# Kernel tuning notes

Measured on AMD Instinct MI355X. Metric: run time of the kernel, lower is better.

The kernel has to match this reference:

```python
import jax, jax.numpy as jnp
import numpy as np

N_E = 1792      # 7 * 256, forced by n_e // 7 == 256 slice width
E_DIM = 64
BETA = 0.25
SUB = 256       # sub-codebook size selected by pos


def setup_inputs() -> dict:
    key = jax.random.key(0)
    k1, k2, k3 = jax.random.split(key, 3)
    z = jax.random.normal(k1, (16, 16384, E_DIM), dtype=jnp.float32)
    one_hot = jax.random.normal(k2, (7,), dtype=jnp.float32)
    W = jax.random.uniform(k3, (N_E, E_DIM), dtype=jnp.float32,
                           minval=-1.0 / N_E, maxval=1.0 / N_E)
    return {"z": z, "one_hot": one_hot, "W": W}


def reference(z, one_hot, W):
    B, T, D = z.shape
    zf = z.reshape(-1, D)                      # [N, D]
    pos = jnp.argmax(one_hot)                  # which 256-entry sub-codebook
    E = jax.lax.dynamic_slice(W, (pos * SUB, 0), (SUB, D))  # [256, D]

    # pairwise squared distances: ||z||^2 + ||e||^2 - 2 z.e
    d = (jnp.sum(zf * zf, axis=1, keepdims=True)
         + jnp.sum(E * E, axis=1)
         - 2.0 * zf @ E.T)                     # [N, 256]
    idx = jnp.argmin(d, axis=1)                # [N]

    # quantize: one-hot @ E == gather (same math, no [N,256] one-hot in HBM)
    z_q = E[idx].reshape(z.shape)              # [B, T, D]

    sg = jax.lax.stop_gradient
    loss = (BETA * jnp.mean((sg(z_q) - z) ** 2)
            + jnp.mean((z_q - sg(z)) ** 2))

    z_q_st = z + sg(z_q - z)                   # straight-through

    # e_mean = column mean of the one-hot matrix == normalized bincount
    counts = jax.ops.segment_sum(jnp.ones_like(idx, jnp.float32), idx,
                                 num_segments=SUB)
    e_mean = counts / idx.shape[0]
    perplexity = jnp.exp(-jnp.sum(e_mean * jnp.log(e_mean + 1e-10)))

    z_q_out = jnp.transpose(z_q_st, (0, 2, 1))  # [B, D, T]
    return (z_q_out, loss, perplexity, idx[:, None])
```

## Files before the change

### kernel.cpp

```cpp
#include <hip/hip_runtime.h>

#define NROWS (16*16384)
#define NJ 256
#define NBLK 1024
#define OUT_LOSS 16777216
#define OUT_PERP 16777217
#define OUT_IDX  16777218

typedef float f32x4  __attribute__((ext_vector_type(4)));
typedef float f32x16 __attribute__((ext_vector_type(16)));
typedef short s16x8  __attribute__((ext_vector_type(8)));

__device__ inline unsigned short f2bf(float f){
  unsigned u = __builtin_bit_cast(unsigned, f);
  unsigned r = (u + 0x7FFFu + ((u >> 16) & 1u)) >> 16;
  return (unsigned short)r;
}
__device__ inline float bf2f(unsigned short h){
  unsigned u = ((unsigned)h) << 16;
  return __builtin_bit_cast(float, u);
}


__global__ __launch_bounds__(512, 2) void vq_main(
    const float* __restrict__ z, const float* __restrict__ oh,
    const float* __restrict__ W, float* __restrict__ out,
    double* __restrict__ lossA, int* __restrict__ wsCnt4,
    unsigned* __restrict__ qn, unsigned* __restrict__ qrows, unsigned segcap)
{
  __shared__ short e1l[NJ*64];
  __shared__ short e2l[NJ*64];
  __shared__ float enl[NJ];
  __shared__ unsigned hist[NJ];
  __shared__ double sLoss[8];
  __shared__ unsigned qn_lds;

  float mv = oh[0]; int pos = 0;
  #pragma unroll
  for (int i = 1; i < 7; i++){ float v = oh[i]; if (v > mv){ mv = v; pos = i; } }

  const int tid = threadIdx.x;

  {
    const int j = tid >> 1, half = tid & 1;
    const float* Wr = W + (size_t)(pos*NJ + j)*64;
    double en = 0.0;
    #pragma unroll
    for (int s4 = 0; s4 < 4; s4++){
      const int s = half*4 + s4;
      f32x4 a = *(const f32x4*)(Wr + s*8);
      f32x4 b = *(const f32x4*)(Wr + s*8 + 4);
      s16x8 p1, p2;
      #pragma unroll
      for (int i = 0; i < 8; i++){
        float vv = (i < 4) ? a[i] : b[i-4];
        unsigned short x1 = f2bf(vv);
        float rr = vv - bf2f(x1);
        p1[i] = (short)x1;
        p2[i] = (short)f2bf(rr);
        en += (double)vv * (double)vv;
      }
      const int slot = s ^ (j & 7);
      *(s16x8*)(e1l + j*64 + slot*8) = p1;
      *(s16x8*)(e2l + j*64 + slot*8) = p2;
    }
    en += __shfl_xor(en, 1);
    if (half == 0) enl[j] = (float)en;
    if (tid < NJ) hist[tid] = 0u;
    if (tid == 0) qn_lds = 0u;
  }
  __syncthreads();

  const int w   = tid >> 6;
  const int l   = tid & 63;
  const int l31 = l & 31;
  const int lh  = l >> 5;

  const int r    = (int)blockIdx.x * 256 + w*32 + l31;
  const int b_i  = r >> 14;
  const int t    = r & 16383;
  const float* zr = z + (size_t)r * 64;

  f32x16 acc[8] = {};
  float zzp = 0.0f;
  #pragma unroll
  for (int ks = 0; ks < 4; ks++){
    const int k0 = ks*16 + lh*8;
    f32x4 za = *(const f32x4*)(zr + k0);
    f32x4 zb = *(const f32x4*)(zr + k0 + 4);
    s16x8 z1f, z2f;
    #pragma unroll
    for (int i = 0; i < 8; i++){
      float vv = (i < 4) ? za[i] : zb[i-4];
      zzp = fmaf(vv, vv, zzp);
      unsigned short x1 = f2bf(vv);
      float rr = vv - bf2f(x1);
      z1f[i] = (short)x1;
      z2f[i] = (short)f2bf(rr);
    }
    #pragma unroll
    for (int jt = 0; jt < 8; jt++){
      const int jrow = jt*32 + l31;
      const int slot = (ks*2 + lh) ^ (jrow & 7);
      const s16x8 e1f = *(const s16x8*)(e1l + jrow*64 + slot*8);
      const s16x8 e2f = *(const s16x8*)(e2l + jrow*64 + slot*8);
      acc[jt] = __builtin_amdgcn_mfma_f32_32x32x16_bf16(e1f, z1f, acc[jt], 0, 0, 0);
      acc[jt] = __builtin_amdgcn_mfma_f32_32x32x16_bf16(e1f, z2f, acc[jt], 0, 0, 0);
      acc[jt] = __builtin_amdgcn_mfma_f32_32x32x16_bf16(e2f, z1f, acc[jt], 0, 0, 0);
    }
  }
  const float zz = zzp + __shfl_xor(zzp, 32);

  float m1 = 3.4e38f, m2 = 3.4e38f; int j1 = 0;
  #pragma unroll
  for (int jt = 0; jt < 8; jt++){
    #pragma unroll
    for (int rq = 0; rq < 4; rq++){
      f32x4 en4 = *(const f32x4*)(enl + jt*32 + rq*8 + lh*4);
      #pragma unroll
      for (int q = 0; q < 4; q++){
        const int reg = rq*4 + q;
        float s  = fmaf(-2.0f, acc[jt][reg], en4[q]);
        int   jj = jt*32 + q + 8*rq + 4*lh;
        bool  lt = s < m1;
        m2 = fminf(m2, lt ? m1 : s);
        j1 = lt ? jj : j1;
        m1 = fminf(m1, s);
      }
    }
  }
  {
    float om1 = __shfl_xor(m1, 32);
    float om2 = __shfl_xor(m2, 32);
    int   oj1 = __shfl_xor(j1, 32);
    float nm2 = fminf(fminf(m2, om2), fmaxf(m1, om1));
    if (om1 < m1 || (om1 == m1 && oj1 < j1)){ m1 = om1; j1 = oj1; }
    m2 = nm2;
  }

  {
    float zs = zz*1.02f + 0.1f;
    float ub = __builtin_bit_cast(float,
                 __builtin_bit_cast(unsigned, zs) & 0x7F800000u) * 1.1920929e-7f;
    float thr = 2.0f*ub + 1.0e-6f;
    if ((m2 - m1 <= thr) && lh == 0){
      unsigned slot = atomicAdd(&qn_lds, 1u);
      if (slot < segcap)
        qrows[(size_t)blockIdx.x*segcap + slot] = (unsigned)r | ((unsigned)j1 << 18);
    }
  }

  if (lh == 0){
    out[(size_t)OUT_IDX + r] = (float)j1;
    atomicAdd(&hist[j1], 1u);
  }
  double lsum = 0.0;
  {
    const float* Er = W + (size_t)(pos*NJ + j1)*64;
    float* zq = out + (size_t)b_i * 1048576 + t;
    #pragma unroll
    for (int ks = 0; ks < 4; ks++){
      const int d0 = ks*16 + lh*8;
      f32x4 ea = *(const f32x4*)(Er + d0);
      f32x4 eb = *(const f32x4*)(Er + d0 + 4);
      f32x4 za = *(const f32x4*)(zr + d0);
      f32x4 zb = *(const f32x4*)(zr + d0 + 4);
      #pragma unroll
      for (int i = 0; i < 8; i++){
        float e  = (i < 4) ? ea[i] : eb[i-4];
        float zv = (i < 4) ? za[i] : zb[i-4];
        float df = e - zv;
        lsum = fma((double)df, (double)df, lsum);
        zq[(size_t)(d0 + i) * 16384] = zv + df;
      }
    }
  }
  #pragma unroll
  for (int off = 1; off < 64; off <<= 1) lsum += __shfl_xor(lsum, off);
  if (l == 0) sLoss[w] = lsum;
  __syncthreads();

  if (tid == 0){
    double bs = 0.0;
    #pragma unroll
    for (int i = 0; i < 8; i++) bs += sLoss[i];
    lossA[blockIdx.x] = bs;
    qn[blockIdx.x] = min(qn_lds, segcap);
  }
  if (tid < NJ){
    unsigned c = hist[tid];
    if (c) atomicAdd(wsCnt4 + ((blockIdx.x & 3) * NJ) + tid, (int)c);
  }
}

__global__ __launch_bounds__(256, 2) void vq_rescue(
    const float* __restrict__ z, const float* __restrict__ oh,
    const float* __restrict__ W, float* __restrict__ out,
    double* __restrict__ lossB, int* __restrict__ wsCnt4,
    const unsigned* __restrict__ qn, const unsigned* __restrict__ qrows,
    unsigned segcap)
{
  #pragma clang fp contract(off)
  __shared__ float elds[NJ*64];
  __shared__ float eeb[NJ];

  float mvv = oh[0]; int pos = 0;
  #pragma unroll
  for (int i = 1; i < 7; i++){ float v = oh[i]; if (v > mvv){ mvv = v; pos = i; } }
  const float* E = W + (size_t)pos * (NJ*64);

  const int tid = threadIdx.x;
  {
    const float* er = E + (size_t)tid * 64;
    float p8[8];
    #pragma unroll
    for (int k = 0; k < 8; k++){
      float ev = er[k];
      elds[tid*64 + (k ^ (tid & 31))] = ev;
      p8[k] = ev*ev;
    }
    #pragma unroll
    for (int k = 8; k < 64; k++){
      float ev = er[k];
      elds[tid*64 + (k ^ (tid & 31))] = ev;
      p8[k & 7] += ev*ev;
    }
    eeb[tid] = ((p8[0]+p8[1])+(p8[2]+p8[3]))+((p8[4]+p8[5])+(p8[6]+p8[7]));
  }
  __syncthreads();

  const int wv = tid >> 6, l = tid & 63;
  const int x  = l & 31;
  const unsigned wgid = blockIdx.x*4u + (unsigned)wv;
  const unsigned seg  = wgid >> 1;
  const unsigned sub  = wgid & 1u;
  const unsigned n    = min(qn[seg], segcap);

  double rloss = 0.0;

  for (unsigned i = sub; i < n; i += 2){
    const unsigned v = qrows[(size_t)seg*segcap + i];
    const int r    = __builtin_amdgcn_readfirstlane((int)(v & 0x3FFFFu));
    const int jold = __builtin_amdgcn_readfirstlane((int)((v >> 18) & 0xFFu));
    const float* zr = z + (size_t)r * 64;

    float zk[64];
    #pragma unroll
    for (int k = 0; k < 64; k++) zk[k] = zr[k];

    float r8[8];
    #pragma unroll
    for (int k = 0; k < 8; k++){ float p = zk[k]*zk[k]; r8[k] = p; }
    #pragma unroll
    for (int k = 8; k < 64; k++){ float p = zk[k]*zk[k]; r8[k & 7] += p; }
    const float zzs = ((r8[0]+r8[1])+(r8[2]+r8[3]))+((r8[4]+r8[5])+(r8[6]+r8[7]));

    float dbest = 3.4e38f; int jbest = 0;
    #pragma unroll
    for (int q = 0; q < 4; q++){
      const int j = l + 64*q;
      float dot = 0.0f;
      #pragma unroll
      for (int k = 0; k < 64; k++){
        float ev = elds[j*64 + (k ^ x)];
        dot = fmaf(ev, zk[k], dot);
      }
      float A  = zzs + eeb[j];
      float tw = 2.0f*dot;
      float d  = A - tw;
      if (d < dbest){ dbest = d; jbest = j; }
    }
    #pragma unroll
    for (int off = 32; off > 0; off >>= 1){
      float od = __shfl_xor(dbest, off);
      int   oj = __shfl_xor(jbest, off);
      if (od < dbest || (od == dbest && oj < jbest)){ dbest = od; jbest = oj; }
    }

    if (jbest != jold){
      const int b_i = r >> 14;
      const int t   = r & 16383;
      const float* en_ = E + (size_t)jbest * 64;
      const float* eo_ = E + (size_t)jold  * 64;
      float ze  = zr[l];
      float dfn = en_[l] - ze;
      float dfo = eo_[l] - ze;
      out[(size_t)b_i * 1048576 + (size_t)l * 16384 + t] = ze + dfn;
      double dl = (double)dfn*(double)dfn - (double)dfo*(double)dfo;
      #pragma unroll
      for (int off = 1; off < 64; off <<= 1) dl += __shfl_xor(dl, off);
      rloss += dl;
      if (l == 0){
        out[(size_t)OUT_IDX + r] = (float)jbest;
        atomicAdd(wsCnt4 + jold,  -1);
        atomicAdd(wsCnt4 + jbest,  1);
      }
    }
  }
  if (l == 0) lossB[wgid] = rloss;
}

__global__ __launch_bounds__(1024) void vq_fin(
    const double* __restrict__ lossA, const double* __restrict__ lossB,
    const int* __restrict__ wsCnt4, float* __restrict__ out)
{
  __shared__ double sh[1024];
  __shared__ double sent[NJ];
  const int t = threadIdx.x;

  sh[t] = lossA[t] + lossB[t] + lossB[1024 + t];
  __syncthreads();
  for (int st = 512; st > 0; st >>= 1){
    if (t < st) sh[t] += sh[t + st];
    __syncthreads();
  }
  if (t < NJ){
    int c = wsCnt4[t] + wsCnt4[256+t] + wsCnt4[512+t] + wsCnt4[768+t];
    double em = (double)c / (double)NROWS;
    sent[t] = em * log(em + 1e-10);
  }
  __syncthreads();
  for (int st = 128; st > 0; st >>= 1){
    if (t < st) sent[t] += sent[t + st];
    __syncthreads();
  }
  if (t == 0){
    out[OUT_LOSS] = (float)(1.25 * (sh[0] / 16777216.0));
    out[OUT_PERP] = (float)exp(-sent[0]);
  }
}

extern "C" void kernel_launch(void* const* d_in, const int* in_sizes, int n_in,
                              void* d_out, int out_size, void* d_ws, size_t ws_size,
                              hipStream_t stream)
{
  const float* z  = (const float*)d_in[0];
  const float* oh = (const float*)d_in[1];
  const float* W  = (const float*)d_in[2];
  float* out = (float*)d_out;

  char* ws = (char*)d_ws;
  int*      wsCnt4 = (int*)(ws + 0);
  unsigned* qn     = (unsigned*)(ws + 4096);
  double*   lossA  = (double*)(ws + 8192);
  double*   lossB  = (double*)(ws + 16384);
  unsigned* qrows  = (unsigned*)(ws + 32768);

  unsigned segcap = 0;
  if (ws_size > 32768 + 4096){
    size_t cap = (ws_size - 32768) / (1024 * 4);
    segcap = (unsigned)(cap > 256 ? 256 : cap);
  }

  hipMemsetAsync(d_ws, 0, 4096, stream);
  vq_main<<<dim3(NBLK), dim3(512), 0, stream>>>(z, oh, W, out, lossA, wsCnt4,
                                                qn, qrows, segcap);
  vq_rescue<<<dim3(512), dim3(256), 0, stream>>>(z, oh, W, out, lossB, wsCnt4,
                                                 qn, qrows, segcap);
  vq_fin<<<dim3(1), dim3(1024), 0, stream>>>(lossA, lossB, wsCnt4, out);
}
```

Measured before the change: 204.6 us.

## Fuse near-tie rescue into main kernel with candidate lists and persistent blocks

After: 176.2 us. 13.9% less time.

```diff
diff --git a/kernel.cpp b/kernel.cpp
--- a/kernel.cpp
+++ b/kernel.cpp
@@ -2,7 +2,6 @@
 
 #define NROWS (16*16384)
 #define NJ 256
-#define NBLK 1024
 #define OUT_LOSS 16777216
 #define OUT_PERP 16777217
 #define OUT_IDX  16777218
@@ -11,35 +10,38 @@
 typedef float f32x16 __attribute__((ext_vector_type(16)));
 typedef short s16x8  __attribute__((ext_vector_type(8)));
 
-__device__ inline unsigned short f2bf(float f){
-  unsigned u = __builtin_bit_cast(unsigned, f);
-  unsigned r = (u + 0x7FFFu + ((u >> 16) & 1u)) >> 16;
-  return (unsigned short)r;
-}
-__device__ inline float bf2f(unsigned short h){
-  unsigned u = ((unsigned)h) << 16;
-  return __builtin_bit_cast(float, u);
-}
-
 
 __global__ __launch_bounds__(512, 2) void vq_main(
     const float* __restrict__ z, const float* __restrict__ oh,
     const float* __restrict__ W, float* __restrict__ out,
-    double* __restrict__ lossA, int* __restrict__ wsCnt4,
-    unsigned* __restrict__ qn, unsigned* __restrict__ qrows, unsigned segcap)
+    double* __restrict__ lossA, int* __restrict__ wsCnt4)
 {
+  #pragma clang fp contract(off)
   __shared__ short e1l[NJ*64];
   __shared__ short e2l[NJ*64];
   __shared__ float enl[NJ];
   __shared__ unsigned hist[NJ];
   __shared__ double sLoss[8];
-  __shared__ unsigned qn_lds;
+  __shared__ int cand[8][32][8];
+  __shared__ unsigned ccnt[8][32];
 
   float mv = oh[0]; int pos = 0;
   #pragma unroll
   for (int i = 1; i < 7; i++){ float v = oh[i]; if (v > mv){ mv = v; pos = i; } }
 
   const int tid = threadIdx.x;
+  const int w = tid >> 6, l = tid & 63, l31 = l & 31, lh = l >> 5;
+  const int rbase = (int)blockIdx.x*1024 + w*32 + l31;
+
+  f32x4 zv[8];
+  {
+    const float* zr = z + (size_t)rbase * 64;
+    #pragma unroll
+    for (int ks = 0; ks < 4; ks++){
+      zv[2*ks]   = *(const f32x4*)(zr + ks*16 + lh*8);
+      zv[2*ks+1] = *(const f32x4*)(zr + ks*16 + lh*8 + 4);
+    }
+  }
 
   {
     const int j = tid >> 1, half = tid & 1;
@@ -49,15 +51,15 @@
     for (int s4 = 0; s4 < 4; s4++){
       const int s = half*4 + s4;
       f32x4 a = *(const f32x4*)(Wr + s*8);
-      f32x4 b = *(const f32x4*)(Wr + s*8 + 4);
+      f32x4 bq = *(const f32x4*)(Wr + s*8 + 4);
       s16x8 p1, p2;
       #pragma unroll
       for (int i = 0; i < 8; i++){
-        float vv = (i < 4) ? a[i] : b[i-4];
-        unsigned short x1 = f2bf(vv);
-        float rr = vv - bf2f(x1);
-        p1[i] = (short)x1;
-        p2[i] = (short)f2bf(rr);
+        float vv = (i < 4) ? a[i] : bq[i-4];
+        unsigned ub = __builtin_bit_cast(unsigned, vv);
+        float rr = vv - __builtin_bit_cast(float, ub & 0xFFFF0000u);
+        p1[i] = (short)(unsigned short)(ub >> 16);
+        p2[i] = (short)(unsigned short)(__builtin_bit_cast(unsigned, rr) >> 16);
         en += (double)vv * (double)vv;
       }
       const int slot = s ^ (j & 7);
@@ -67,125 +69,189 @@
     en += __shfl_xor(en, 1);
     if (half == 0) enl[j] = (float)en;
     if (tid < NJ) hist[tid] = 0u;
-    if (tid == 0) qn_lds = 0u;
   }
   __syncthreads();
 
-  const int w   = tid >> 6;
-  const int l   = tid & 63;
-  const int l31 = l & 31;
-  const int lh  = l >> 5;
-
-  const int r    = (int)blockIdx.x * 256 + w*32 + l31;
-  const int b_i  = r >> 14;
-  const int t    = r & 16383;
-  const float* zr = z + (size_t)r * 64;
-
-  f32x16 acc[8] = {};
-  float zzp = 0.0f;
-  #pragma unroll
-  for (int ks = 0; ks < 4; ks++){
-    const int k0 = ks*16 + lh*8;
-    f32x4 za = *(const f32x4*)(zr + k0);
-    f32x4 zb = *(const f32x4*)(zr + k0 + 4);
-    s16x8 z1f, z2f;
-    #pragma unroll
-    for (int i = 0; i < 8; i++){
-      float vv = (i < 4) ? za[i] : zb[i-4];
-      zzp = fmaf(vv, vv, zzp);
-      unsigned short x1 = f2bf(vv);
-      float rr = vv - bf2f(x1);
-      z1f[i] = (short)x1;
-      z2f[i] = (short)f2bf(rr);
-    }
+  double lsum = 0.0;
+
+  #pragma unroll 1
+  for (int b = 0; b < 4; b++){
+    const int r    = rbase + b*256;
+    const int b_i  = r >> 14;
+    const int t    = r & 16383;
+    const float* zr = z + (size_t)r * 64;
+
+    float zzp = 0.0f;
+    s16x8 z1f[4], z2f[4];
+    #pragma unroll
+    for (int ks = 0; ks < 4; ks++){
+      #pragma unroll
+      for (int i = 0; i < 8; i++){
+        float vv = (i < 4) ? zv[2*ks][i] : zv[2*ks+1][i-4];
+        zzp = fmaf(vv, vv, zzp);
+        unsigned ub = __builtin_bit_cast(unsigned, vv);
+        float rr = vv - __builtin_bit_cast(float, ub & 0xFFFF0000u);
+        z1f[ks][i] = (short)(unsigned short)(ub >> 16);
+        z2f[ks][i] = (short)(unsigned short)(__builtin_bit_cast(unsigned, rr) >> 16);
+      }
+    }
+    const float zz = zzp + __shfl_xor(zzp, 32);
+
+    f32x16 acc[8] = {};
+    #pragma unroll
+    for (int ks = 0; ks < 4; ks++){
+      #pragma unroll
+      for (int jt = 0; jt < 8; jt++){
+        const int jrow = jt*32 + l31;
+        const int slot = (ks*2 + lh) ^ (jrow & 7);
+        const s16x8 e1f = *(const s16x8*)(e1l + jrow*64 + slot*8);
+        const s16x8 e2f = *(const s16x8*)(e2l + jrow*64 + slot*8);
+        acc[jt] = __builtin_amdgcn_mfma_f32_32x32x16_bf16(e1f, z1f[ks], acc[jt], 0, 0, 0);
+        acc[jt] = __builtin_amdgcn_mfma_f32_32x32x16_bf16(e1f, z2f[ks], acc[jt], 0, 0, 0);
+        acc[jt] = __builtin_amdgcn_mfma_f32_32x32x16_bf16(e2f, z1f[ks], acc[jt], 0, 0, 0);
+      }
+    }
+
+    float m1 = 3.4e38f, m2 = 3.4e38f; int j1 = 0;
     #pragma unroll
     for (int jt = 0; jt < 8; jt++){
-      const int jrow = jt*32 + l31;
-      const int slot = (ks*2 + lh) ^ (jrow & 7);
-      const s16x8 e1f = *(const s16x8*)(e1l + jrow*64 + slot*8);
-      const s16x8 e2f = *(const s16x8*)(e2l + jrow*64 + slot*8);
-      acc[jt] = __builtin_amdgcn_mfma_f32_32x32x16_bf16(e1f, z1f, acc[jt], 0, 0, 0);
-      acc[jt] = __builtin_amdgcn_mfma_f32_32x32x16_bf16(e1f, z2f, acc[jt], 0, 0, 0);
-      acc[jt] = __builtin_amdgcn_mfma_f32_32x32x16_bf16(e2f, z1f, acc[jt], 0, 0, 0);
-    }
-  }
-  const float zz = zzp + __shfl_xor(zzp, 32);
-
-  float m1 = 3.4e38f, m2 = 3.4e38f; int j1 = 0;
-  #pragma unroll
-  for (int jt = 0; jt < 8; jt++){
-    #pragma unroll
-    for (int rq = 0; rq < 4; rq++){
-      f32x4 en4 = *(const f32x4*)(enl + jt*32 + rq*8 + lh*4);
-      #pragma unroll
-      for (int q = 0; q < 4; q++){
-        const int reg = rq*4 + q;
-        float s  = fmaf(-2.0f, acc[jt][reg], en4[q]);
-        int   jj = jt*32 + q + 8*rq + 4*lh;
-        bool  lt = s < m1;
-        m2 = fminf(m2, lt ? m1 : s);
-        j1 = lt ? jj : j1;
-        m1 = fminf(m1, s);
-      }
-    }
-  }
-  {
-    float om1 = __shfl_xor(m1, 32);
-    float om2 = __shfl_xor(m2, 32);
-    int   oj1 = __shfl_xor(j1, 32);
-    float nm2 = fminf(fminf(m2, om2), fmaxf(m1, om1));
-    if (om1 < m1 || (om1 == m1 && oj1 < j1)){ m1 = om1; j1 = oj1; }
-    m2 = nm2;
-  }
-
-  {
+      #pragma unroll
+      for (int rq = 0; rq < 4; rq++){
+        f32x4 en4 = *(const f32x4*)(enl + jt*32 + rq*8 + lh*4);
+        #pragma unroll
+        for (int q = 0; q < 4; q++){
+          float s  = fmaf(-2.0f, acc[jt][rq*4+q], en4[q]);
+          int   jj = jt*32 + q + 8*rq + 4*lh;
+          bool  lt = s < m1;
+          m2 = fminf(m2, lt ? m1 : s);
+          j1 = lt ? jj : j1;
+          m1 = fminf(m1, s);
+        }
+      }
+    }
+    {
+      float om1 = __shfl_xor(m1, 32);
+      float om2 = __shfl_xor(m2, 32);
+      int   oj1 = __shfl_xor(j1, 32);
+      float nm2 = fminf(fminf(m2, om2), fmaxf(m1, om1));
+      if (om1 < m1 || (om1 == m1 && oj1 < j1)){ m1 = om1; j1 = oj1; }
+      m2 = nm2;
+    }
+
     float zs = zz*1.02f + 0.1f;
     float ub = __builtin_bit_cast(float,
                  __builtin_bit_cast(unsigned, zs) & 0x7F800000u) * 1.1920929e-7f;
-    float thr = 2.0f*ub + 1.0e-6f;
-    if ((m2 - m1 <= thr) && lh == 0){
-      unsigned slot = atomicAdd(&qn_lds, 1u);
-      if (slot < segcap)
-        qrows[(size_t)blockIdx.x*segcap + slot] = (unsigned)r | ((unsigned)j1 << 18);
-    }
-  }
-
-  if (lh == 0){
-    out[(size_t)OUT_IDX + r] = (float)j1;
-    atomicAdd(&hist[j1], 1u);
-  }
-  double lsum = 0.0;
-  {
-    const float* Er = W + (size_t)(pos*NJ + j1)*64;
-    float* zq = out + (size_t)b_i * 1048576 + t;
-    #pragma unroll
-    for (int ks = 0; ks < 4; ks++){
-      const int d0 = ks*16 + lh*8;
-      f32x4 ea = *(const f32x4*)(Er + d0);
-      f32x4 eb = *(const f32x4*)(Er + d0 + 4);
-      f32x4 za = *(const f32x4*)(zr + d0);
-      f32x4 zb = *(const f32x4*)(zr + d0 + 4);
-      #pragma unroll
-      for (int i = 0; i < 8; i++){
-        float e  = (i < 4) ? ea[i] : eb[i-4];
-        float zv = (i < 4) ? za[i] : zb[i-4];
-        float df = e - zv;
-        lsum = fma((double)df, (double)df, lsum);
-        zq[(size_t)(d0 + i) * 16384] = zv + df;
-      }
-    }
-  }
+    const float thr = 2.0f*ub + 4.0e-6f;
+    const bool flag = (m2 - m1 <= thr);
+    if (lh == 0) ccnt[w][l31] = 0u;
+    if (flag){
+      #pragma unroll
+      for (int jt = 0; jt < 8; jt++){
+        #pragma unroll
+        for (int rq = 0; rq < 4; rq++){
+          f32x4 en4 = *(const f32x4*)(enl + jt*32 + rq*8 + lh*4);
+          #pragma unroll
+          for (int q = 0; q < 4; q++){
+            float s = fmaf(-2.0f, acc[jt][rq*4+q], en4[q]);
+            if (s <= m1 + thr){
+              unsigned u = atomicAdd(&ccnt[w][l31], 1u);
+              if (u < 8) cand[w][l31][u] = jt*32 + q + 8*rq + 4*lh;
+            }
+          }
+        }
+      }
+    }
+
+    if (b < 3){
+      const float* zn = z + (size_t)(r + 256) * 64;
+      #pragma unroll
+      for (int ks = 0; ks < 4; ks++){
+        zv[2*ks]   = *(const f32x4*)(zn + ks*16 + lh*8);
+        zv[2*ks+1] = *(const f32x4*)(zn + ks*16 + lh*8 + 4);
+      }
+    }
+
+    unsigned rowmask = (unsigned)(__ballot(flag) & 0xFFFFFFFFull);
+    while (rowmask){
+      const int fr = __builtin_ctz(rowmask); rowmask &= rowmask - 1;
+      const int rrow = (int)blockIdx.x*1024 + b*256 + w*32 + fr;
+      const float* zr2 = z + (size_t)rrow * 64;
+      unsigned ncu = ccnt[w][fr]; int nc = (int)(ncu > 8u ? 8u : ncu);
+
+      float r8[8];
+      #pragma unroll
+      for (int k = 0; k < 8; k++){ float p = zr2[k]*zr2[k]; r8[k] = p; }
+      #pragma unroll
+      for (int k = 8; k < 64; k++){ float p = zr2[k]*zr2[k]; r8[k & 7] += p; }
+      const float zzs = ((r8[0]+r8[1])+(r8[2]+r8[3]))+((r8[4]+r8[5])+(r8[6]+r8[7]));
+
+      float dbest = 3.4e38f; int jbest = 1 << 20;
+      if (l < nc){
+        const int jc = cand[w][fr][l];
+        const float* er = W + (size_t)(pos*NJ + jc)*64;
+        float dot = 0.0f; float s8[8];
+        #pragma unroll
+        for (int k = 0; k < 8; k++){
+          float ev = er[k];
+          dot = fmaf(ev, zr2[k], dot);
+          s8[k] = ev*ev;
+        }
+        #pragma unroll
+        for (int k = 8; k < 64; k++){
+          float ev = er[k];
+          dot = fmaf(ev, zr2[k], dot);
+          s8[k & 7] += ev*ev;
+        }
+        float ee = ((s8[0]+s8[1])+(s8[2]+s8[3]))+((s8[4]+s8[5])+(s8[6]+s8[7]));
+        float A  = zzs + ee;
+        float tw = 2.0f*dot;
+        dbest = A - tw;
+        jbest = jc;
+      }
+      #pragma unroll
+      for (int off = 32; off > 0; off >>= 1){
+        float od = __shfl_xor(dbest, off);
+        int   oj = __shfl_xor(jbest, off);
+        if (od < dbest || (od == dbest && oj < jbest)){ dbest = od; jbest = oj; }
+      }
+      if (l31 == fr) j1 = jbest;
+    }
+
+    if (lh == 0){
+      out[(size_t)OUT_IDX + r] = (float)j1;
+      atomicAdd(&hist[j1], 1u);
+    }
+    {
+      const float* Er = W + (size_t)(pos*NJ + j1)*64;
+      float* zq = out + (size_t)b_i * 1048576 + t;
+      #pragma unroll
+      for (int ks = 0; ks < 4; ks++){
+        const int d0 = ks*16 + lh*8;
+        f32x4 ea = *(const f32x4*)(Er + d0);
+        f32x4 eb = *(const f32x4*)(Er + d0 + 4);
+        f32x4 za = *(const f32x4*)(zr + d0);
+        f32x4 zb = *(const f32x4*)(zr + d0 + 4);
+        #pragma unroll
+        for (int i = 0; i < 8; i++){
+          float e  = (i < 4) ? ea[i] : eb[i-4];
+          float zx = (i < 4) ? za[i] : zb[i-4];
+          float df = e - zx;
+          lsum = fma((double)df, (double)df, lsum);
+          zq[(size_t)(d0 + i) * 16384] = zx + df;
+        }
+      }
+    }
+  }
+
   #pragma unroll
   for (int off = 1; off < 64; off <<= 1) lsum += __shfl_xor(lsum, off);
   if (l == 0) sLoss[w] = lsum;
   __syncthreads();
-
   if (tid == 0){
     double bs = 0.0;
     #pragma unroll
     for (int i = 0; i < 8; i++) bs += sLoss[i];
     lossA[blockIdx.x] = bs;
-    qn[blockIdx.x] = min(qn_lds, segcap);
   }
   if (tid < NJ){
     unsigned c = hist[tid];
@@ -193,135 +259,20 @@
   }
 }
 
-__global__ __launch_bounds__(256, 2) void vq_rescue(
-    const float* __restrict__ z, const float* __restrict__ oh,
-    const float* __restrict__ W, float* __restrict__ out,
-    double* __restrict__ lossB, int* __restrict__ wsCnt4,
-    const unsigned* __restrict__ qn, const unsigned* __restrict__ qrows,
-    unsigned segcap)
+__global__ void vq_fin(const double* __restrict__ lossA,
+                       const int* __restrict__ wsCnt4,
+                       float* __restrict__ out)
 {
-  #pragma clang fp contract(off)
-  __shared__ float elds[NJ*64];
-  __shared__ float eeb[NJ];
-
-  float mvv = oh[0]; int pos = 0;
-  #pragma unroll
-  for (int i = 1; i < 7; i++){ float v = oh[i]; if (v > mvv){ mvv = v; pos = i; } }
-  const float* E = W + (size_t)pos * (NJ*64);
-
-  const int tid = threadIdx.x;
-  {
-    const float* er = E + (size_t)tid * 64;
-    float p8[8];
-    #pragma unroll
-    for (int k = 0; k < 8; k++){
-      float ev = er[k];
-      elds[tid*64 + (k ^ (tid & 31))] = ev;
-      p8[k] = ev*ev;
-    }
-    #pragma unroll
-    for (int k = 8; k < 64; k++){
-      float ev = er[k];
-      elds[tid*64 + (k ^ (tid & 31))] = ev;
-      p8[k & 7] += ev*ev;
-    }
-    eeb[tid] = ((p8[0]+p8[1])+(p8[2]+p8[3]))+((p8[4]+p8[5])+(p8[6]+p8[7]));
-  }
-  __syncthreads();
-
-  const int wv = tid >> 6, l = tid & 63;
-  const int x  = l & 31;
-  const unsigned wgid = blockIdx.x*4u + (unsigned)wv;
-  const unsigned seg  = wgid >> 1;
-  const unsigned sub  = wgid & 1u;
-  const unsigned n    = min(qn[seg], segcap);
-
-  double rloss = 0.0;
-
-  for (unsigned i = sub; i < n; i += 2){
-    const unsigned v = qrows[(size_t)seg*segcap + i];
-    const int r    = __builtin_amdgcn_readfirstlane((int)(v & 0x3FFFFu));
-    const int jold = __builtin_amdgcn_readfirstlane((int)((v >> 18) & 0xFFu));
-    const float* zr = z + (size_t)r * 64;
-
-    float zk[64];
-    #pragma unroll
-    for (int k = 0; k < 64; k++) zk[k] = zr[k];
-
-    float r8[8];
-    #pragma unroll
-    for (int k = 0; k < 8; k++){ float p = zk[k]*zk[k]; r8[k] = p; }
-    #pragma unroll
-    for (int k = 8; k < 64; k++){ float p = zk[k]*zk[k]; r8[k & 7] += p; }
-    const float zzs = ((r8[0]+r8[1])+(r8[2]+r8[3]))+((r8[4]+r8[5])+(r8[6]+r8[7]));
-
-    float dbest = 3.4e38f; int jbest = 0;
-    #pragma unroll
-    for (int q = 0; q < 4; q++){
-      const int j = l + 64*q;
-      float dot = 0.0f;
-      #pragma unroll
-      for (int k = 0; k < 64; k++){
-        float ev = elds[j*64 + (k ^ x)];
-        dot = fmaf(ev, zk[k], dot);
-      }
-      float A  = zzs + eeb[j];
-      float tw = 2.0f*dot;
-      float d  = A - tw;
-      if (d < dbest){ dbest = d; jbest = j; }
-    }
-    #pragma unroll
-    for (int off = 32; off > 0; off >>= 1){
-      float od = __shfl_xor(dbest, off);
-      int   oj = __shfl_xor(jbest, off);
-      if (od < dbest || (od == dbest && oj < jbest)){ dbest = od; jbest = oj; }
-    }
-
-    if (jbest != jold){
-      const int b_i = r >> 14;
-      const int t   = r & 16383;
-      const float* en_ = E + (size_t)jbest * 64;
-      const float* eo_ = E + (size_t)jold  * 64;
-      float ze  = zr[l];
-      float dfn = en_[l] - ze;
-      float dfo = eo_[l] - ze;
-      out[(size_t)b_i * 1048576 + (size_t)l * 16384 + t] = ze + dfn;
-      double dl = (double)dfn*(double)dfn - (double)dfo*(double)dfo;
-      #pragma unroll
-      for (int off = 1; off < 64; off <<= 1) dl += __shfl_xor(dl, off);
-      rloss += dl;
-      if (l == 0){
-        out[(size_t)OUT_IDX + r] = (float)jbest;
-        atomicAdd(wsCnt4 + jold,  -1);
-        atomicAdd(wsCnt4 + jbest,  1);
-      }
-    }
-  }
-  if (l == 0) lossB[wgid] = rloss;
-}
-
-__global__ __launch_bounds__(1024) void vq_fin(
-    const double* __restrict__ lossA, const double* __restrict__ lossB,
-    const int* __restrict__ wsCnt4, float* __restrict__ out)
-{
-  __shared__ double sh[1024];
+  __shared__ double sh[NJ];
   __shared__ double sent[NJ];
   const int t = threadIdx.x;
-
-  sh[t] = lossA[t] + lossB[t] + lossB[1024 + t];
+  sh[t] = lossA[t];
+  int c = wsCnt4[t] + wsCnt4[256+t] + wsCnt4[512+t] + wsCnt4[768+t];
+  double em = (double)c / (double)NROWS;
+  sent[t] = em * log(em + 1e-10);
   __syncthreads();
-  for (int st = 512; st > 0; st >>= 1){
-    if (t < st) sh[t] += sh[t + st];
-    __syncthreads();
-  }
-  if (t < NJ){
-    int c = wsCnt4[t] + wsCnt4[256+t] + wsCnt4[512+t] + wsCnt4[768+t];
-    double em = (double)c / (double)NROWS;
-    sent[t] = em * log(em + 1e-10);
-  }
-  __syncthreads();
-  for (int st = 128; st > 0; st >>= 1){
-    if (t < st) sent[t] += sent[t + st];
+  for (int s = 128; s > 0; s >>= 1){
+    if (t < s){ sh[t] += sh[t + s]; sent[t] += sent[t + s]; }
     __syncthreads();
   }
   if (t == 0){
@@ -340,22 +291,10 @@
   float* out = (float*)d_out;
 
   char* ws = (char*)d_ws;
-  int*      wsCnt4 = (int*)(ws + 0);
-  unsigned* qn     = (unsigned*)(ws + 4096);
-  double*   lossA  = (double*)(ws + 8192);
-  double*   lossB  = (double*)(ws + 16384);
-  unsigned* qrows  = (unsigned*)(ws + 32768);
-
-  unsigned segcap = 0;
-  if (ws_size > 32768 + 4096){
-    size_t cap = (ws_size - 32768) / (1024 * 4);
-    segcap = (unsigned)(cap > 256 ? 256 : cap);
-  }
+  int*    wsCnt4 = (int*)(ws + 0);
+  double* lossA  = (double*)(ws + 4096);
 
   hipMemsetAsync(d_ws, 0, 4096, stream);
-  vq_main<<<dim3(NBLK), dim3(512), 0, stream>>>(z, oh, W, out, lossA, wsCnt4,
-                                                qn, qrows, segcap);
-  vq_rescue<<<dim3(512), dim3(256), 0, stream>>>(z, oh, W, out, lossB, wsCnt4,
-                                                 qn, qrows, segcap);
-  vq_fin<<<dim3(1), dim3(1024), 0, stream>>>(lossA, lossB, wsCnt4, out);
+  vq_main<<<dim3(256), dim3(512), 0, stream>>>(z, oh, W, out, lossA, wsCnt4);
+  vq_fin<<<dim3(1), dim3(256), 0, stream>>>(lossA, wsCnt4, out);
 }
```
